# Kernel optimization log

Measured on AMD Instinct MI355X. Metric: run time of the kernel, lower is better.

## Reference

```python
import jax, jax.numpy as jnp
import numpy as np

B, D = 8192, 128
MARGIN = 0.1
N_CLASSES, N_GROUPS = 64, 8


def setup_inputs() -> dict:
    key = jax.random.key(0)
    k1, k2, k3 = jax.random.split(key, 3)
    embeddings = jax.random.normal(k1, (B, D), dtype=jnp.float32)
    labels = jax.random.randint(k2, (B,), 0, N_CLASSES, dtype=jnp.int64)
    groups = jax.random.randint(k3, (B,), 0, N_GROUPS, dtype=jnp.int64)
    return {"embeddings": embeddings, "labels": labels, "groups": groups}


def reference(embeddings, labels, groups):
    # cosine metric: L2-normalize rows (torch F.normalize eps=1e-12)
    norm = jnp.maximum(jnp.linalg.norm(embeddings, axis=1, keepdims=True), 1e-12)
    x = embeddings / norm
    dist = 1.0 - jnp.matmul(x, x.T)                      # [B, B]

    n = embeddings.shape[0]
    eye = jnp.eye(n, dtype=bool)
    same_label = labels[:, None] == labels[None, :]       # [B, B]
    pos_mask = same_label & ~eye
    neg_mask = ~same_label
    neg_sg_mask = neg_mask & (groups[:, None] == groups[None, :])

    BIG = jnp.float32(1e9)
    # hardest positive per row (masked max), hardest negative per row (masked min)
    dist_ap = jnp.max(jnp.where(pos_mask, dist, -BIG), axis=1)
    dist_an_sg = jnp.min(jnp.where(neg_sg_mask, dist, BIG), axis=1)
    dist_an_all = jnp.min(jnp.where(neg_mask, dist, BIG), axis=1)

    has_pos = jnp.any(pos_mask, axis=1)
    has_neg_sg = jnp.any(neg_sg_mask, axis=1)
    has_neg = jnp.any(neg_mask, axis=1)

    # fallback: same-group negatives preferred, else any negative
    dist_an = jnp.where(has_neg_sg, dist_an_sg, dist_an_all)

    loss = jax.nn.relu(dist_ap - dist_an + MARGIN)        # [B]
    # original only averages strictly-positive losses over valid anchors
    include = has_pos & has_neg & (loss > 0)
    cnt = jnp.sum(include.astype(jnp.float32))
    total = jnp.sum(jnp.where(include, loss, 0.0))
    final = jnp.where(cnt > 0, total / jnp.maximum(cnt, 1.0), 0.0)
    final = jnp.where(jnp.isnan(final), 0.0, final)
    return final
```

## Files before the change

kernel.cpp:

```cpp
#include <hip/hip_runtime.h>
#include <math.h>

#define NB 8192
#define DK 128
#define IT 128
#define JT 64
#define SPLITJ 16
#define JSPAN (NB / SPLITJ)
#define NT (JSPAN / JT)
#define BSTRH 136

typedef __attribute__((ext_vector_type(8))) short short8;
typedef __attribute__((ext_vector_type(16))) float float16;

__device__ inline unsigned short f2bf(float f) {
    unsigned int x = __float_as_uint(f);
    unsigned int r = (x + 0x7fffu + ((x >> 16) & 1u)) >> 16;
    return (unsigned short)r;
}

__global__ void norm_kernel(const float* __restrict__ emb, const int* __restrict__ labels,
                            const int* __restrict__ groups, unsigned short* __restrict__ xnb,
                            int* __restrict__ meta) {
    int row  = blockIdx.x * 4 + (threadIdx.x >> 6);
    int lane = threadIdx.x & 63;
    float2 v = ((const float2*)(emb + (size_t)row * DK))[lane];
    float ss = v.x * v.x + v.y * v.y;
#pragma unroll
    for (int off = 32; off; off >>= 1) ss += __shfl_xor(ss, off, 64);
    float inv = 1.0f / fmaxf(sqrtf(ss), 1e-12f);
    ushort2 o;
    o.x = f2bf(v.x * inv);
    o.y = f2bf(v.y * inv);
    ((ushort2*)(xnb + (size_t)row * DK))[lane] = o;
    if (lane == 0) meta[row] = (labels[row] << 8) | groups[row];
}

__global__ __launch_bounds__(256, 2) void mine_mfma(
    const unsigned short* __restrict__ xnb, const int* __restrict__ meta,
    float* __restrict__ ap_part, float* __restrict__ ansg_part,
    float* __restrict__ anall_part) {
    __shared__ unsigned short Bs[2][JT * BSTRH];

    const int tid  = threadIdx.x;
    const int w    = tid >> 6;
    const int lane = tid & 63;
    const int half = lane >> 5;
    const int l31  = lane & 31;
    const int i0    = blockIdx.x * IT;
    const int jbase = blockIdx.y * JSPAN;
    const int irow  = i0 + w * 32;

    short8 afrag[8];
#pragma unroll
    for (int ks = 0; ks < 8; ks++)
        afrag[ks] = *(const short8*)(xnb + (size_t)(irow + l31) * DK + ks * 16 + half * 8);

    int metaI[16];
    float apS[16], ansgS[16], anallS[16];
#pragma unroll
    for (int reg = 0; reg < 16; reg++) {
        int r = (reg & 3) + 8 * (reg >> 2) + 4 * half;
        metaI[reg] = meta[irow + r];
        apS[reg] = 1e9f; ansgS[reg] = -1e9f; anallS[reg] = -1e9f;
    }

#pragma unroll
    for (int s = 0; s < 4; s++) {
        int chunk = tid + s * 256;
        int row = chunk >> 4, k4 = chunk & 15;
        *(uint4*)&Bs[0][row * BSTRH + k4 * 8] =
            *(const uint4*)(xnb + (size_t)(jbase + row) * DK + k4 * 8);
    }
    __syncthreads();

    const float BIG = 1e9f, NEG = -1e9f;

    for (int jt = 0; jt < NT; jt++) {
        const int cur = jt & 1;
        const int j0  = jbase + jt * JT;

        uint4 pre[4];
        if (jt + 1 < NT) {
            const int j0n = j0 + JT;
#pragma unroll
            for (int s = 0; s < 4; s++) {
                int chunk = tid + s * 256;
                int row = chunk >> 4, k4 = chunk & 15;
                pre[s] = *(const uint4*)(xnb + (size_t)(j0n + row) * DK + k4 * 8);
            }
        }

        int mjc[2];
        mjc[0] = meta[j0 + l31];
        mjc[1] = meta[j0 + 32 + l31];

#pragma unroll
        for (int ct = 0; ct < 2; ct++) {
            float16 c;
#pragma unroll
            for (int e = 0; e < 16; e++) c[e] = 0.0f;

            const int bro = ct * 32 + l31;
#pragma unroll
            for (int ks = 0; ks < 8; ks++) {
                short8 b = *(const short8*)&Bs[cur][bro * BSTRH + ks * 16 + half * 8];
                c = __builtin_amdgcn_mfma_f32_32x32x16_bf16(afrag[ks], b, c, 0, 0, 0);
            }

            const int mj = mjc[ct];
#pragma unroll
            for (int reg = 0; reg < 16; reg++) {
                float s = c[reg];
                int x = metaI[reg] ^ mj;
                bool sl = (unsigned)x < 0x100u;
                float selap = sl ? s : BIG;
                apS[reg] = fminf(apS[reg], selap);
                float selna = sl ? NEG : s;
                anallS[reg] = fmaxf(anallS[reg], selna);
                bool sg = (x & 0xFF) == 0;
                float selsg = sg ? selna : NEG;
                ansgS[reg] = fmaxf(ansgS[reg], selsg);
            }
        }

        if (jt + 1 < NT) {
#pragma unroll
            for (int s = 0; s < 4; s++) {
                int chunk = tid + s * 256;
                int row = chunk >> 4, k4 = chunk & 15;
                *(uint4*)&Bs[cur ^ 1][row * BSTRH + k4 * 8] = pre[s];
            }
        }
        __syncthreads();
    }

#pragma unroll
    for (int reg = 0; reg < 16; reg++) {
#pragma unroll
        for (int off = 16; off; off >>= 1) {
            apS[reg]    = fminf(apS[reg],    __shfl_xor(apS[reg],    off, 64));
            ansgS[reg]  = fmaxf(ansgS[reg],  __shfl_xor(ansgS[reg],  off, 64));
            anallS[reg] = fmaxf(anallS[reg], __shfl_xor(anallS[reg], off, 64));
        }
    }
    if (l31 == 0) {
#pragma unroll
        for (int reg = 0; reg < 16; reg++) {
            int r = (reg & 3) + 8 * (reg >> 2) + 4 * half;
            size_t idx = (size_t)blockIdx.y * NB + (irow + r);
            ap_part[idx]    = apS[reg];
            ansg_part[idx]  = ansgS[reg];
            anall_part[idx] = anallS[reg];
        }
    }
}

__global__ void combine_kernel(const float* __restrict__ ap_part,
                               const float* __restrict__ ansg_part,
                               const float* __restrict__ anall_part,
                               float* __restrict__ bsum, float* __restrict__ bcnt) {
    int i = blockIdx.x * 256 + threadIdx.x;
    float apS = 1e9f, asg = -1e9f, aall = -1e9f;
#pragma unroll
    for (int h = 0; h < SPLITJ; h++) {
        size_t idx = (size_t)h * NB + i;
        apS  = fminf(apS,  ap_part[idx]);
        asg  = fmaxf(asg,  ansg_part[idx]);
        aall = fmaxf(aall, anall_part[idx]);
    }
    float anS = (asg > -1e8f) ? asg : aall;
    float loss = anS - apS + 0.1f;
    float inc = (loss > 0.0f) ? 1.0f : 0.0f;
    float val = inc * loss;

    __shared__ float ssum[4], scnt[4];
#pragma unroll
    for (int off = 32; off; off >>= 1) {
        val += __shfl_xor(val, off, 64);
        inc += __shfl_xor(inc, off, 64);
    }
    int wid = threadIdx.x >> 6, lane = threadIdx.x & 63;
    if (lane == 0) { ssum[wid] = val; scnt[wid] = inc; }
    __syncthreads();
    if (threadIdx.x == 0) {
        float s = 0.f, c = 0.f;
#pragma unroll
        for (int wv = 0; wv < 4; wv++) { s += ssum[wv]; c += scnt[wv]; }
        bsum[blockIdx.x] = s;
        bcnt[blockIdx.x] = c;
    }
}

#define NCOMB (NB / 256)

__global__ void finalize_kernel(const float* __restrict__ bsum,
                                const float* __restrict__ bcnt,
                                float* __restrict__ out) {
    int lane = threadIdx.x;
    float s = (lane < NCOMB) ? bsum[lane] : 0.0f;
    float c = (lane < NCOMB) ? bcnt[lane] : 0.0f;
#pragma unroll
    for (int off = 32; off; off >>= 1) {
        s += __shfl_xor(s, off, 64);
        c += __shfl_xor(c, off, 64);
    }
    if (lane == 0) {
        float r = (c > 0.0f) ? s / fmaxf(c, 1.0f) : 0.0f;
        if (isnan(r)) r = 0.0f;
        out[0] = r;
    }
}

extern "C" void kernel_launch(void* const* d_in, const int* in_sizes, int n_in,
                              void* d_out, int out_size, void* d_ws, size_t ws_size,
                              hipStream_t stream) {
    const float* emb  = (const float*)d_in[0];
    const int* labels = (const int*)d_in[1];
    const int* groups = (const int*)d_in[2];
    float* out = (float*)d_out;

    unsigned short* xnb = (unsigned short*)d_ws;
    int*   meta       = (int*)(xnb + (size_t)NB * DK);
    float* ap_part    = (float*)(meta + NB);
    float* ansg_part  = ap_part + (size_t)SPLITJ * NB;
    float* anall_part = ansg_part + (size_t)SPLITJ * NB;
    float* bsum       = anall_part + (size_t)SPLITJ * NB;
    float* bcnt       = bsum + NCOMB;

    norm_kernel<<<NB / 4, 256, 0, stream>>>(emb, labels, groups, xnb, meta);
    mine_mfma<<<dim3(NB / IT, SPLITJ), 256, 0, stream>>>(
        xnb, meta, ap_part, ansg_part, anall_part);
    combine_kernel<<<NB / 256, 256, 0, stream>>>(ap_part, ansg_part, anall_part, bsum, bcnt);
    finalize_kernel<<<1, 64, 0, stream>>>(bsum, bcnt, out);
}
```

Before: 118.4 us.

## Encode mining masks as offsets to cut reductions, fuse finalize via atomics

The per-pair masked min/max mining is re-encoded with additive offsets on the cosine similarity. Positives are shifted by -8 and same-group entries by +4, so one max tracks the hardest same-group-or-any negative and a second max tracks the hardest positive. This drops one accumulator array, several selects per element and one partial-output buffer, and the launch bound is raised to 3 blocks per SM. The finalize kernel is folded into combine using atomic accumulation and a last-block ticket, which adds a memset and relies on float atomics and on the offsets separating the similarity ranges.

```diff
diff --git a/kernel.cpp b/kernel.cpp
--- a/kernel.cpp
+++ b/kernel.cpp
@@ -9,6 +9,7 @@
 #define JSPAN (NB / SPLITJ)
 #define NT (JSPAN / JT)
 #define BSTRH 136
+#define NCOMB (NB / 256)
 
 typedef __attribute__((ext_vector_type(8))) short short8;
 typedef __attribute__((ext_vector_type(16))) float float16;
@@ -36,10 +37,9 @@
     if (lane == 0) meta[row] = (labels[row] << 8) | groups[row];
 }
 
-__global__ __launch_bounds__(256, 2) void mine_mfma(
+__global__ __launch_bounds__(256, 3) void mine_mfma(
     const unsigned short* __restrict__ xnb, const int* __restrict__ meta,
-    float* __restrict__ ap_part, float* __restrict__ ansg_part,
-    float* __restrict__ anall_part) {
+    float* __restrict__ ap_part, float* __restrict__ an_part) {
     __shared__ unsigned short Bs[2][JT * BSTRH];
 
     const int tid  = threadIdx.x;
@@ -57,12 +57,12 @@
         afrag[ks] = *(const short8*)(xnb + (size_t)(irow + l31) * DK + ks * 16 + half * 8);
 
     int metaI[16];
-    float apS[16], ansgS[16], anallS[16];
+    float apn[16], anc[16];
 #pragma unroll
     for (int reg = 0; reg < 16; reg++) {
         int r = (reg & 3) + 8 * (reg >> 2) + 4 * half;
         metaI[reg] = meta[irow + r];
-        apS[reg] = 1e9f; ansgS[reg] = -1e9f; anallS[reg] = -1e9f;
+        apn[reg] = -1e9f; anc[reg] = -1e9f;
     }
 
 #pragma unroll
@@ -74,8 +74,6 @@
     }
     __syncthreads();
 
-    const float BIG = 1e9f, NEG = -1e9f;
-
     for (int jt = 0; jt < NT; jt++) {
         const int cur = jt & 1;
         const int j0  = jbase + jt * JT;
@@ -114,13 +112,13 @@
                 float s = c[reg];
                 int x = metaI[reg] ^ mj;
                 bool sl = (unsigned)x < 0x100u;
-                float selap = sl ? s : BIG;
-                apS[reg] = fminf(apS[reg], selap);
-                float selna = sl ? NEG : s;
-                anallS[reg] = fmaxf(anallS[reg], selna);
-                bool sg = (x & 0xFF) == 0;
-                float selsg = sg ? selna : NEG;
-                ansgS[reg] = fmaxf(ansgS[reg], selsg);
+                float t8 = s - 8.0f;
+                float t  = sl ? t8 : s;
+                apn[reg] = fmaxf(apn[reg], -t);
+                bool sg = (x & 0xFFu) == 0u;
+                float t4 = t + 4.0f;
+                float v  = sg ? t4 : t;
+                anc[reg] = fmaxf(anc[reg], v);
             }
         }
 
@@ -139,9 +137,8 @@
     for (int reg = 0; reg < 16; reg++) {
 #pragma unroll
         for (int off = 16; off; off >>= 1) {
-            apS[reg]    = fminf(apS[reg],    __shfl_xor(apS[reg],    off, 64));
-            ansgS[reg]  = fmaxf(ansgS[reg],  __shfl_xor(ansgS[reg],  off, 64));
-            anallS[reg] = fmaxf(anallS[reg], __shfl_xor(anallS[reg], off, 64));
+            apn[reg] = fmaxf(apn[reg], __shfl_xor(apn[reg], off, 64));
+            anc[reg] = fmaxf(anc[reg], __shfl_xor(anc[reg], off, 64));
         }
     }
     if (l31 == 0) {
@@ -149,28 +146,26 @@
         for (int reg = 0; reg < 16; reg++) {
             int r = (reg & 3) + 8 * (reg >> 2) + 4 * half;
             size_t idx = (size_t)blockIdx.y * NB + (irow + r);
-            ap_part[idx]    = apS[reg];
-            ansg_part[idx]  = ansgS[reg];
-            anall_part[idx] = anallS[reg];
+            ap_part[idx] = apn[reg];
+            an_part[idx] = anc[reg];
         }
     }
 }
 
 __global__ void combine_kernel(const float* __restrict__ ap_part,
-                               const float* __restrict__ ansg_part,
-                               const float* __restrict__ anall_part,
-                               float* __restrict__ bsum, float* __restrict__ bcnt) {
+                               const float* __restrict__ an_part,
+                               float* __restrict__ accum, int* __restrict__ ticket,
+                               float* __restrict__ out) {
     int i = blockIdx.x * 256 + threadIdx.x;
-    float apS = 1e9f, asg = -1e9f, aall = -1e9f;
+    float apn = -1e9f, anc = -1e9f;
 #pragma unroll
     for (int h = 0; h < SPLITJ; h++) {
         size_t idx = (size_t)h * NB + i;
-        apS  = fminf(apS,  ap_part[idx]);
-        asg  = fmaxf(asg,  ansg_part[idx]);
-        aall = fmaxf(aall, anall_part[idx]);
-    }
-    float anS = (asg > -1e8f) ? asg : aall;
-    float loss = anS - apS + 0.1f;
+        apn = fmaxf(apn, ap_part[idx]);
+        anc = fmaxf(anc, an_part[idx]);
+    }
+    float anS = (anc > 2.0f) ? anc - 4.0f : anc;
+    float loss = anS + apn - 7.9f;
     float inc = (loss > 0.0f) ? 1.0f : 0.0f;
     float val = inc * loss;
 
@@ -187,28 +182,18 @@
         float s = 0.f, c = 0.f;
 #pragma unroll
         for (int wv = 0; wv < 4; wv++) { s += ssum[wv]; c += scnt[wv]; }
-        bsum[blockIdx.x] = s;
-        bcnt[blockIdx.x] = c;
-    }
-}
-
-#define NCOMB (NB / 256)
-
-__global__ void finalize_kernel(const float* __restrict__ bsum,
-                                const float* __restrict__ bcnt,
-                                float* __restrict__ out) {
-    int lane = threadIdx.x;
-    float s = (lane < NCOMB) ? bsum[lane] : 0.0f;
-    float c = (lane < NCOMB) ? bcnt[lane] : 0.0f;
-#pragma unroll
-    for (int off = 32; off; off >>= 1) {
-        s += __shfl_xor(s, off, 64);
-        c += __shfl_xor(c, off, 64);
-    }
-    if (lane == 0) {
-        float r = (c > 0.0f) ? s / fmaxf(c, 1.0f) : 0.0f;
-        if (isnan(r)) r = 0.0f;
-        out[0] = r;
+        atomicAdd(&accum[0], s);
+        atomicAdd(&accum[1], c);
+        __threadfence();
+        int old = atomicAdd(ticket, 1);
+        if (old == gridDim.x - 1) {
+            __threadfence();
+            float total = __hip_atomic_load(&accum[0], __ATOMIC_RELAXED, __HIP_MEMORY_SCOPE_AGENT);
+            float cnt   = __hip_atomic_load(&accum[1], __ATOMIC_RELAXED, __HIP_MEMORY_SCOPE_AGENT);
+            float r = (cnt > 0.0f) ? total / fmaxf(cnt, 1.0f) : 0.0f;
+            if (isnan(r)) r = 0.0f;
+            out[0] = r;
+        }
     }
 }
 
@@ -221,16 +206,15 @@
     float* out = (float*)d_out;
 
     unsigned short* xnb = (unsigned short*)d_ws;
-    int*   meta       = (int*)(xnb + (size_t)NB * DK);
-    float* ap_part    = (float*)(meta + NB);
-    float* ansg_part  = ap_part + (size_t)SPLITJ * NB;
-    float* anall_part = ansg_part + (size_t)SPLITJ * NB;
-    float* bsum       = anall_part + (size_t)SPLITJ * NB;
-    float* bcnt       = bsum + NCOMB;
-
+    int*   meta    = (int*)(xnb + (size_t)NB * DK);
+    float* ap_part = (float*)(meta + NB);
+    float* an_part = ap_part + (size_t)SPLITJ * NB;
+    float* accum   = an_part + (size_t)SPLITJ * NB;
+    int*   ticket  = (int*)(accum + 2);
+
+    hipMemsetAsync(accum, 0, 3 * sizeof(float), stream);
     norm_kernel<<<NB / 4, 256, 0, stream>>>(emb, labels, groups, xnb, meta);
     mine_mfma<<<dim3(NB / IT, SPLITJ), 256, 0, stream>>>(
-        xnb, meta, ap_part, ansg_part, anall_part);
-    combine_kernel<<<NB / 256, 256, 0, stream>>>(ap_part, ansg_part, anall_part, bsum, bcnt);
-    finalize_kernel<<<1, 64, 0, stream>>>(bsum, bcnt, out);
-}
+        xnb, meta, ap_part, an_part);
+    combine_kernel<<<NCOMB, 256, 0, stream>>>(ap_part, an_part, accum, ticket, out);
+}
```

Result: faster. 99.09 us (-16.3%).
